# Kernel optimization log

Hardware: AMD Instinct MI355X
Metric: run time of the kernel (lower is better)

## Reference

```python
import jax, jax.numpy as jnp
import numpy as np

B_SZ, SEQ, D_MODEL, D_STATE, KSIZE = 8, 4096, 1024, 64, 64
DT_MIN, DT_MAX = 0.001, 0.1


def setup_inputs() -> dict:
    key = jax.random.key(0)
    k1, k2, k3, k4 = jax.random.split(key, 4)
    u = jax.random.normal(k1, (B_SZ, SEQ, D_MODEL), dtype=jnp.float32)
    # HiPPO-like init: A = -(n+1)
    A = -(jnp.arange(D_STATE, dtype=jnp.float32) + 1.0)
    Bp = 0.01 * jax.random.normal(k2, (D_STATE, D_MODEL), dtype=jnp.float32)
    Cp = 0.01 * jax.random.normal(k3, (D_MODEL, D_STATE), dtype=jnp.float32)
    Dp = jnp.ones((D_MODEL,), dtype=jnp.float32)
    log_dt = jnp.log(jax.random.uniform(k4, (D_MODEL,), dtype=jnp.float32,
                                        minval=DT_MIN, maxval=DT_MAX))
    return {"u": u, "A": A, "B": Bp, "C": Cp, "D": Dp, "log_dt": log_dt}


def reference(u, A, B, C, D, log_dt):
    # u: (batch, seq_len, d_model)
    batch, seq_len, d_model = u.shape
    L = min(seq_len, KSIZE)  # truncated SSM kernel length

    # --- SSM kernel (same math as ssm_kernel) ---
    dt = jnp.exp(log_dt)                         # (d_model,)
    A_bar = jnp.exp(A[:, None] * dt[None, :])    # (d_state, d_model)
    powers = jnp.arange(L)[:, None, None]        # (L,1,1)
    A_powers = A_bar[None, :, :] ** powers       # (L, d_state, d_model)
    # K[l,k] = sum_{m,d} C[m,d] * A_bar[d,k]^l * B[d,k]  (faithful to original einsum)
    K = jnp.einsum('md,ldk,dk->lk', C, A_powers, B)  # (L, d_model)

    # --- Batched per-channel 'same' convolution via FFT ---
    # Equivalent to jnp.convolve(u[b,:,i], K[:,i], mode='same') for every b, i,
    # with L <= seq_len so the 'same' slice starts at (L-1)//2.
    n = seq_len + L - 1
    Uf = jnp.fft.rfft(u, n=n, axis=1)            # (batch, nf, d_model)
    Kf = jnp.fft.rfft(K, n=n, axis=0)            # (nf, d_model)
    conv_full = jnp.fft.irfft(Uf * Kf[None], n=n, axis=1)  # (batch, n, d_model)
    start = (L - 1) // 2
    y = conv_full[:, start:start + seq_len, :]

    # skip connection
    y = y + D[None, None, :] * u
    return y
```

## Files before the change

### kernel.cpp

```cpp
#include <hip/hip_runtime.h>

#define SEQ 4096
#define DM 1024
#define DS 64
#define KS 64

#define TCH 64
#define TT  128
#define R   16
#define NROW (TT + 64)

typedef const __attribute__((address_space(1))) void* gas_ptr;
typedef __attribute__((address_space(3))) void* las_ptr;
__device__ __forceinline__ void async_cp16(const void* g, void* s) {
    __builtin_amdgcn_global_load_lds((gas_ptr)g, (las_ptr)s, 16, 0, 0);
}

__global__ void csum_kernel(const float* __restrict__ C, float* __restrict__ csum) {
    int d    = threadIdx.x & 63;
    int mloc = threadIdx.x >> 6;
    int m0   = blockIdx.x * 64;
    float s = 0.f;
#pragma unroll
    for (int j = 0; j < 16; ++j)
        s += C[(m0 + j * 4 + mloc) * DS + d];
    __shared__ float red[4][64];
    red[mloc][d] = s;
    __syncthreads();
    if (threadIdx.x < 64) {
        float t = red[0][d] + red[1][d] + red[2][d] + red[3][d];
        atomicAdd(&csum[d], t);
    }
}

__global__ void taps_kernel(const float* __restrict__ A, const float* __restrict__ B,
                            const float* __restrict__ log_dt,
                            const float* __restrict__ csum, float* __restrict__ Ktl) {
    int g = blockIdx.x * blockDim.x + threadIdx.x;
    int k = g & (DM - 1);
    int l = g >> 10;
    float dt = __expf(log_dt[k]);
    float fl = (float)l;
    float acc = 0.f;
#pragma unroll 8
    for (int d = 0; d < DS; ++d)
        acc += csum[d] * __expf(A[d] * dt * fl) * B[d * DM + k];
    Ktl[g] = acc;
}

__global__ __launch_bounds__(256, 2)
void conv_kernel(const float* __restrict__ u, const float* __restrict__ Ktl,
                 const float* __restrict__ D, float* __restrict__ y) {
    __shared__ __align__(16) float smem_u[NROW * TCH];
    __shared__ __align__(16) float smem_t[KS * TCH];

    int k0 = blockIdx.x * TCH;
    int t0 = blockIdx.y * TT;
    int b  = blockIdx.z;

    int lane = threadIdx.x & 63;
    int wv   = threadIdx.x >> 6;

    const float* gt = u + (size_t)b * SEQ * DM + (size_t)(t0 - 32) * DM + k0;

    bool interior = (blockIdx.y > 0) && (blockIdx.y + 1 < SEQ / TT);

#pragma unroll
    for (int j = 0; j < 4; ++j) {
        int fb = j * 4096 + wv * 1024;
        int f  = fb + lane * 16;
        int l  = f >> 8;
        int c  = (f & 255) >> 2;
        async_cp16(Ktl + l * DM + k0 + c, (char*)smem_t + fb);
    }

    if (interior) {
#pragma unroll
        for (int j = 0; j < 12; ++j) {
            int fb = j * 4096 + wv * 1024;
            int f  = fb + lane * 16;
            int r  = f >> 8;
            int c  = (f & 255) >> 2;
            async_cp16(gt + (size_t)r * DM + c, (char*)smem_u + fb);
        }
    } else {
#pragma unroll
        for (int j = 0; j < 12; ++j) {
            int f = j * 4096 + threadIdx.x * 16;
            int r = f >> 8;
            int c = (f & 255) >> 2;
            int t = t0 - 32 + r;
            float4 v = make_float4(0.f, 0.f, 0.f, 0.f);
            if (t >= 0 && t < SEQ)
                v = *(const float4*)(gt + (size_t)r * DM + c);
            *(float4*)((char*)smem_u + f) = v;
        }
    }
    __syncthreads();

    int c2 = threadIdx.x & 31;
    int tg = threadIdx.x >> 5;
    int ts = t0 + tg * R;
    int rb = tg * R;

    const float2* us = (const float2*)smem_u;
    const float2* tp = (const float2*)smem_t;

    float2 acc[R];
#pragma unroll
    for (int r = 0; r < R; ++r) acc[r] = make_float2(0.f, 0.f);

    float2 w[31];
#pragma unroll
    for (int i = 0; i < 31; ++i) w[i] = us[(rb + 48 + i) * 32 + c2];

    float2 D2 = *(const float2*)(D + k0 + 2 * c2);

#pragma unroll
    for (int c = 0; c < 4; ++c) {
        if (c > 0) {
#pragma unroll
            for (int i = 30; i >= 16; --i) w[i] = w[i - 16];
#pragma unroll
            for (int i = 0; i < 16; ++i) w[i] = us[(rb + 48 - 16 * c + i) * 32 + c2];
        }
        if (c == 1) {
#pragma unroll
            for (int r = 0; r < R; ++r) {
                acc[r].x = fmaf(D2.x, w[r].x, acc[r].x);
                acc[r].y = fmaf(D2.y, w[r].y, acc[r].y);
            }
        }
#pragma unroll
        for (int j = 0; j < 16; ++j) {
            float2 t2 = tp[(16 * c + j) * 32 + c2];
#pragma unroll
            for (int r = 0; r < R; ++r) {
                acc[r].x = fmaf(t2.x, w[r + 15 - j].x, acc[r].x);
                acc[r].y = fmaf(t2.y, w[r + 15 - j].y, acc[r].y);
            }
        }
    }

    float2* yp2 = (float2*)y + (size_t)b * SEQ * (DM / 2) + (size_t)ts * (DM / 2) + (k0 >> 1) + c2;
#pragma unroll
    for (int r = 0; r < R; ++r)
        yp2[(size_t)r * (DM / 2)] = acc[r];
}

extern "C" void kernel_launch(void* const* d_in, const int* in_sizes, int n_in,
                              void* d_out, int out_size, void* d_ws, size_t ws_size,
                              hipStream_t stream) {
    const float* u      = (const float*)d_in[0];
    const float* A      = (const float*)d_in[1];
    const float* Bp     = (const float*)d_in[2];
    const float* Cp     = (const float*)d_in[3];
    const float* Dp     = (const float*)d_in[4];
    const float* log_dt = (const float*)d_in[5];
    float* y = (float*)d_out;

    float* csum = (float*)d_ws;
    float* Ktl  = csum + 64;

    hipMemsetAsync(csum, 0, DS * sizeof(float), stream);
    csum_kernel<<<16, 256, 0, stream>>>(Cp, csum);
    taps_kernel<<<(DM * KS) / 256, 256, 0, stream>>>(A, Bp, log_dt, csum, Ktl);

    dim3 grid(DM / TCH, SEQ / TT, 8);
    conv_kernel<<<grid, 256, 0, stream>>>(u, Ktl, Dp, y);
}
```

Baseline: 268.8 us.

## Halve time tile and use rolling 16-entry window for convolution inputs

Halves the per-block time tile (TT 128→64) and rows per thread (R 16→8), shrinking LDS use and raising the occupancy hint to three blocks per SIMD. The input window is rewritten from a 31-register array refilled in four chunks into a 16-entry ring buffer that loads one new row per tap. This cuts register pressure and LDS footprint to allow more concurrent waves. In exchange, each thread reuses each loaded tap across fewer outputs, the 64-row halo becomes a larger share of each tile, and there are more LDS loads per FMA.

```diff
diff --git a/kernel.cpp b/kernel.cpp
--- a/kernel.cpp
+++ b/kernel.cpp
@@ -6,8 +6,8 @@
 #define KS 64
 
 #define TCH 64
-#define TT  128
-#define R   16
+#define TT  64
+#define R   8
 #define NROW (TT + 64)
 
 typedef const __attribute__((address_space(1))) void* gas_ptr;
@@ -48,7 +48,7 @@
     Ktl[g] = acc;
 }
 
-__global__ __launch_bounds__(256, 2)
+__global__ __launch_bounds__(256, 3)
 void conv_kernel(const float* __restrict__ u, const float* __restrict__ Ktl,
                  const float* __restrict__ D, float* __restrict__ y) {
     __shared__ __align__(16) float smem_u[NROW * TCH];
@@ -76,7 +76,7 @@
 
     if (interior) {
 #pragma unroll
-        for (int j = 0; j < 12; ++j) {
+        for (int j = 0; j < 8; ++j) {
             int fb = j * 4096 + wv * 1024;
             int f  = fb + lane * 16;
             int r  = f >> 8;
@@ -85,7 +85,7 @@
         }
     } else {
 #pragma unroll
-        for (int j = 0; j < 12; ++j) {
+        for (int j = 0; j < 8; ++j) {
             int f = j * 4096 + threadIdx.x * 16;
             int r = f >> 8;
             int c = (f & 255) >> 2;
@@ -110,35 +110,33 @@
 #pragma unroll
     for (int r = 0; r < R; ++r) acc[r] = make_float2(0.f, 0.f);
 
-    float2 w[31];
-#pragma unroll
-    for (int i = 0; i < 31; ++i) w[i] = us[(rb + 48 + i) * 32 + c2];
-
     float2 D2 = *(const float2*)(D + k0 + 2 * c2);
 
+    float2 w[16];
 #pragma unroll
-    for (int c = 0; c < 4; ++c) {
-        if (c > 0) {
+    for (int m = 55; m <= 70; ++m)
+        w[m & 15] = us[(rb + m) * 32 + c2];
+
 #pragma unroll
-            for (int i = 30; i >= 16; --i) w[i] = w[i - 16];
+    for (int l = 0; l < 64; ++l) {
+        float2 t2 = tp[l * 32 + c2];
 #pragma unroll
-            for (int i = 0; i < 16; ++i) w[i] = us[(rb + 48 - 16 * c + i) * 32 + c2];
+        for (int r = 0; r < R; ++r) {
+            float2 uv = w[(r + 63 - l) & 15];
+            acc[r].x = fmaf(t2.x, uv.x, acc[r].x);
+            acc[r].y = fmaf(t2.y, uv.y, acc[r].y);
         }
-        if (c == 1) {
+        if (l == 31) {
 #pragma unroll
             for (int r = 0; r < R; ++r) {
-                acc[r].x = fmaf(D2.x, w[r].x, acc[r].x);
-                acc[r].y = fmaf(D2.y, w[r].y, acc[r].y);
+                float2 uv = w[(r + 32) & 15];
+                acc[r].x = fmaf(D2.x, uv.x, acc[r].x);
+                acc[r].y = fmaf(D2.y, uv.y, acc[r].y);
             }
         }
-#pragma unroll
-        for (int j = 0; j < 16; ++j) {
-            float2 t2 = tp[(16 * c + j) * 32 + c2];
-#pragma unroll
-            for (int r = 0; r < R; ++r) {
-                acc[r].x = fmaf(t2.x, w[r + 15 - j].x, acc[r].x);
-                acc[r].y = fmaf(t2.y, w[r + 15 - j].y, acc[r].y);
-            }
+        if (l <= 54) {
+            int m = 54 - l;
+            w[m & 15] = us[(rb + m) * 32 + c2];
         }
     }
 
```

Measured after the change: 256.1 us. 4.7% less time.
